# Kernel tuning notes

Hardware: AMD Instinct MI355X
Metric: run time of the kernel (lower is better)

## Reference

```python
import jax, jax.numpy as jnp
import numpy as np

B, N, C, H = 8, 1024, 1024, 16
DH = C // H
SCALE = DH ** -0.5
EPS = 1e-6


def layernorm(x, g, b):
    m = jnp.mean(x, axis=-1, keepdims=True)
    v = jnp.mean(jnp.square(x - m), axis=-1, keepdims=True)
    return (x - m) * jax.lax.rsqrt(v + EPS) * g + b


def setup_inputs() -> dict:
    key = jax.random.key(0)
    ks = jax.random.split(key, 5)
    w = 0.02  # init std for weights, keeps activations sane
    return {
        "x": jax.random.normal(ks[0], (B, N, C), jnp.float32),
        "qkv_w": jax.random.normal(ks[1], (C, 3 * C), jnp.float32) * w,
        "qkv_b": jnp.zeros((3 * C,), jnp.float32),
        "proj_w": jax.random.normal(ks[2], (C, C), jnp.float32) * w,
        "proj_b": jnp.zeros((C,), jnp.float32),
        "n1_g": jnp.ones((C,), jnp.float32),
        "n1_b": jnp.zeros((C,), jnp.float32),
        "fc1_w": jax.random.normal(ks[3], (C, 4 * C), jnp.float32) * w,
        "fc1_b": jnp.zeros((4 * C,), jnp.float32),
        "fc2_w": jax.random.normal(ks[4], (4 * C, C), jnp.float32) * w,
        "fc2_b": jnp.zeros((C,), jnp.float32),
        "n2_g": jnp.ones((C,), jnp.float32),
        "n2_b": jnp.zeros((C,), jnp.float32),
    }


def reference(x, qkv_w, qkv_b, proj_w, proj_b, n1_g, n1_b,
              fc1_w, fc1_b, fc2_w, fc2_b, n2_g, n2_b):
    # --- manual multi-head attention (timm-style, materializes BxHxNxN) ---
    qkv = x @ qkv_w + qkv_b                                  # [B,N,3C]
    qkv = qkv.reshape(B, N, 3, H, DH).transpose(2, 0, 3, 1, 4)  # [3,B,H,N,DH]
    q, k, v = qkv[0], qkv[1], qkv[2]
    attn = jax.nn.softmax(jnp.einsum('bhnd,bhmd->bhnm', q, k) * SCALE, axis=-1)
    y = jnp.einsum('bhnm,bhmd->bhnd', attn, v)               # [B,H,N,DH]
    y = y.transpose(0, 2, 1, 3).reshape(B, N, C)
    y = y @ proj_w + proj_b                                  # attention output replaces x
    # --- NOTE: unusual block wiring, faithful to source ---
    # x = attn_out; x = x + norm1(x); x = x + norm2(mlp(x))
    y = y + layernorm(y, n1_g, n1_b)
    h = jax.nn.gelu(y @ fc1_w + fc1_b, approximate=False)    # timm Mlp: fc1 -> GELU -> fc2
    h = h @ fc2_w + fc2_b
    y = y + layernorm(h, n2_g, n2_b)
    return y
```

## Files before the change

### kernel.cpp

```cpp
#include <hip/hip_runtime.h>
#include <hip/hip_bf16.h>
#include <math.h>

typedef __bf16 bf16;
typedef __bf16 bf16x8 __attribute__((ext_vector_type(8)));
typedef float f32x4 __attribute__((ext_vector_type(4)));

__device__ __forceinline__ int swz_idx(int row, int col) {
    return ((row) << 6) + (((((col) >> 3) ^ ((row) & 7)) << 3) | ((col) & 7));
}
#define LDS_SWZ8(row, c8) ((((row)) << 6) + ((((c8) ^ ((row) & 7))) << 3))

__device__ __forceinline__ void gload_lds16(const bf16* g, bf16* l) {
    __builtin_amdgcn_global_load_lds(
        (const __attribute__((address_space(1))) void*)g,
        (__attribute__((address_space(3))) void*)l,
        16, 0, 0);
}

template <int ROWS>
__device__ __forceinline__ void stage_swz(const bf16* __restrict__ src, long rstride,
                                          bf16* lds, int tid) {
#pragma unroll
    for (int pass = 0; pass < ROWS / 32; ++pass) {
        int e = pass * 2048 + tid * 8;
        int r = e >> 6;
        int c8 = (e >> 3) & 7;
        int sc8 = c8 ^ (r & 7);
        gload_lds16(src + (long)r * rstride + sc8 * 8, lds + e);
    }
}

__global__ void transpose_cvt(const float* __restrict__ src, bf16* __restrict__ dst,
                              int R, int C) {
    __shared__ float tile[32][33];
    int bx = blockIdx.x * 32;
    int by = blockIdx.y * 32;
    int tx = threadIdx.x, ty = threadIdx.y;
#pragma unroll
    for (int j = 0; j < 32; j += 8)
        tile[ty + j][tx] = src[(long)(by + ty + j) * C + bx + tx];
    __syncthreads();
#pragma unroll
    for (int j = 0; j < 32; j += 8)
        dst[(long)(bx + ty + j) * R + by + tx] = (bf16)tile[tx][ty + j];
}

__global__ void cvt_bf16_kernel(const float* __restrict__ src, bf16* __restrict__ dst,
                                long n) {
    long i = ((long)blockIdx.x * blockDim.x + threadIdx.x) * 4;
    if (i < n) {
        float4 v = *(const float4*)(src + i);
        short4 pk;
        pk.x = (short)__builtin_bit_cast(unsigned short, (bf16)v.x);
        pk.y = (short)__builtin_bit_cast(unsigned short, (bf16)v.y);
        pk.z = (short)__builtin_bit_cast(unsigned short, (bf16)v.z);
        pk.w = (short)__builtin_bit_cast(unsigned short, (bf16)v.w);
        *(short4*)(dst + i) = pk;
    }
}

template <int MODE>
__global__ __launch_bounds__(256, 2)
void gemm_bt(const bf16* __restrict__ A, const bf16* __restrict__ Bt,
             const float* __restrict__ bias,
             float* __restrict__ Cf, bf16* __restrict__ Cb0,
             bf16* __restrict__ Cb1, bf16* __restrict__ Cb2,
             int M, int N, int K) {
    __shared__ __align__(16) bf16 lsA[128 * 64];
    __shared__ __align__(16) bf16 lsB[128 * 64];

    const int tid = threadIdx.x;
    const int lane = tid & 63;
    const int w = tid >> 6;
    const int wm = w >> 1, wn = w & 1;
    const int l15 = lane & 15, l4 = lane >> 4;
    const int row0 = blockIdx.y * 128;
    const int col0 = blockIdx.x * 128;

    f32x4 acc[4][4] = {};

    for (int k0 = 0; k0 < K; k0 += 64) {
        stage_swz<128>(A + (long)row0 * K + k0, K, lsA, tid);
        stage_swz<128>(Bt + (long)col0 * K + k0, K, lsB, tid);
        __syncthreads();
#pragma unroll
        for (int kk = 0; kk < 2; ++kk) {
            int c8 = kk * 4 + l4;
            bf16x8 af[4], bfr[4];
#pragma unroll
            for (int mt = 0; mt < 4; ++mt)
                af[mt] = *(const bf16x8*)(&lsA[LDS_SWZ8(wm * 64 + mt * 16 + l15, c8)]);
#pragma unroll
            for (int nt = 0; nt < 4; ++nt)
                bfr[nt] = *(const bf16x8*)(&lsB[LDS_SWZ8(wn * 64 + nt * 16 + l15, c8)]);
#pragma unroll
            for (int mt = 0; mt < 4; ++mt)
#pragma unroll
                for (int nt = 0; nt < 4; ++nt)
                    acc[mt][nt] = __builtin_amdgcn_mfma_f32_16x16x32_bf16(
                        af[mt], bfr[nt], acc[mt][nt], 0, 0, 0);
        }
        __syncthreads();
    }

#pragma unroll
    for (int mt = 0; mt < 4; ++mt) {
#pragma unroll
        for (int nt = 0; nt < 4; ++nt) {
            int colb = col0 + wn * 64 + nt * 16 + l15;
            float bv = bias[colb];
#pragma unroll
            for (int i = 0; i < 4; ++i) {
                int row = row0 + wm * 64 + mt * 16 + l4 * 4 + i;
                int col = colb;
                float v = acc[mt][nt][i] + bv;
                if (MODE == 0) {
                    int b = row >> 10, nn = row & 1023;
                    int s = col >> 10, rem = col & 1023;
                    int h = rem >> 6, d = rem & 63;
                    long bh = (long)b * 16 + h;
                    if (s == 0)      Cb0[(bh * 1024 + nn) * 64 + d] = (bf16)(v * 0.125f);
                    else if (s == 1) Cb1[(bh * 1024 + nn) * 64 + d] = (bf16)v;
                    else             Cb2[(bh * 64 + d) * 1024 + nn] = (bf16)v;
                } else if (MODE == 1) {
                    Cf[(long)row * N + col] = v;
                } else if (MODE == 2) {
                    float g = 0.5f * v * (1.0f + erff(v * 0.70710678118f));
                    Cb0[(long)row * N + col] = (bf16)g;
                } else {
                    Cf[(long)row * N + col] = v;
                }
            }
        }
    }
}

__global__ __launch_bounds__(256, 2)
void attn_flash(const bf16* __restrict__ Q, const bf16* __restrict__ Kv,
                const bf16* __restrict__ Vt, bf16* __restrict__ Y) {
    __shared__ __align__(16) bf16 lsK[2][64 * 64];
    __shared__ __align__(16) bf16 lsV[2][64 * 64];
    __shared__ __align__(16) bf16 lsP[4][16 * 64];

    const int tid = threadIdx.x;
    const int lane = tid & 63;
    const int w = tid >> 6;
    const int l15 = lane & 15, l4 = lane >> 4;
    const int bh = blockIdx.y;
    const int b = bh >> 4, h = bh & 15;
    const int q0 = blockIdx.x * 64;

    const bf16* qp = Q + ((long)bh * 1024 + q0 + w * 16 + l15) * 64;
    bf16x8 qa[2];
    qa[0] = *(const bf16x8*)(qp + 8 * l4);
    qa[1] = *(const bf16x8*)(qp + 32 + 8 * l4);

    const bf16* kbase = Kv + (long)bh * 1024 * 64;
    const bf16* vbase = Vt + (long)bh * 64 * 1024;

    float lsum[4] = {0.f, 0.f, 0.f, 0.f};
    f32x4 oacc[4] = {};

    stage_swz<64>(kbase, 64, lsK[0], tid);
    stage_swz<64>(vbase, 1024, lsV[0], tid);
    __syncthreads();

    for (int t = 0; t < 16; ++t) {
        const int cur = t & 1;
        if (t < 15) {
            int kv0 = (t + 1) * 64;
            stage_swz<64>(kbase + (long)kv0 * 64, 64, lsK[cur ^ 1], tid);
            stage_swz<64>(vbase + kv0, 1024, lsV[cur ^ 1], tid);
        }

        f32x4 s[4] = {};
#pragma unroll
        for (int kk = 0; kk < 2; ++kk) {
            int c8 = kk * 4 + l4;
#pragma unroll
            for (int nt = 0; nt < 4; ++nt) {
                bf16x8 kb = *(const bf16x8*)(&lsK[cur][LDS_SWZ8(nt * 16 + l15, c8)]);
                s[nt] = __builtin_amdgcn_mfma_f32_16x16x32_bf16(qa[kk], kb, s[nt], 0, 0, 0);
            }
        }

#pragma unroll
        for (int i = 0; i < 4; ++i) {
            int prow = l4 * 4 + i;
#pragma unroll
            for (int nt = 0; nt < 4; ++nt) {
                float p = __expf(s[nt][i]);
                lsum[i] += p;
                lsP[w][swz_idx(prow, nt * 16 + l15)] = (bf16)p;
            }
        }
        __builtin_amdgcn_sched_barrier(0);
        asm volatile("s_waitcnt lgkmcnt(0)" ::: "memory");
        __builtin_amdgcn_sched_barrier(0);

#pragma unroll
        for (int kk = 0; kk < 2; ++kk) {
            int c8 = kk * 4 + l4;
            bf16x8 pa = *(const bf16x8*)(&lsP[w][LDS_SWZ8(l15, c8)]);
#pragma unroll
            for (int nt = 0; nt < 4; ++nt) {
                bf16x8 vb = *(const bf16x8*)(&lsV[cur][LDS_SWZ8(nt * 16 + l15, c8)]);
                oacc[nt] = __builtin_amdgcn_mfma_f32_16x16x32_bf16(pa, vb, oacc[nt], 0, 0, 0);
            }
        }
        __syncthreads();
    }

#pragma unroll
    for (int i = 0; i < 4; ++i) {
#pragma unroll
        for (int off = 1; off < 16; off <<= 1)
            lsum[i] += __shfl_xor(lsum[i], off);
    }

#pragma unroll
    for (int i = 0; i < 4; ++i) {
        float rinv = 1.0f / lsum[i];
        int row = q0 + w * 16 + l4 * 4 + i;
#pragma unroll
        for (int nt = 0; nt < 4; ++nt) {
            int d = nt * 16 + l15;
            Y[((long)b * 1024 + row) * 1024 + h * 64 + d] = (bf16)(oacc[nt][i] * rinv);
        }
    }
}

__device__ __forceinline__ float block_reduce_sum(float v, float* sm) {
#pragma unroll
    for (int off = 1; off < 64; off <<= 1) v += __shfl_xor(v, off);
    int w = threadIdx.x >> 6;
    if ((threadIdx.x & 63) == 0) sm[w] = v;
    __syncthreads();
    v = sm[0] + sm[1] + sm[2] + sm[3];
    __syncthreads();
    return v;
}

__global__ __launch_bounds__(256)
void res_ln(float* __restrict__ Yf, bf16* __restrict__ Yb,
            const float* __restrict__ g, const float* __restrict__ beta) {
    __shared__ float sm[4];
    const long row = blockIdx.x;
    float* p = Yf + row * 1024;
    const int t = threadIdx.x;
    float4 x = *(const float4*)(p + t * 4);
    float s = x.x + x.y + x.z + x.w;
    s = block_reduce_sum(s, sm);
    float mean = s * (1.0f / 1024.0f);
    float d0 = x.x - mean, d1 = x.y - mean, d2 = x.z - mean, d3 = x.w - mean;
    float sq = d0 * d0 + d1 * d1 + d2 * d2 + d3 * d3;
    sq = block_reduce_sum(sq, sm);
    float rs = rsqrtf(sq * (1.0f / 1024.0f) + 1e-6f);
    float4 gg = *(const float4*)(g + t * 4);
    float4 bb = *(const float4*)(beta + t * 4);
    float o0 = x.x + d0 * rs * gg.x + bb.x;
    float o1 = x.y + d1 * rs * gg.y + bb.y;
    float o2 = x.z + d2 * rs * gg.z + bb.z;
    float o3 = x.w + d3 * rs * gg.w + bb.w;
    *(float4*)(p + t * 4) = make_float4(o0, o1, o2, o3);
    short4 pk;
    pk.x = (short)__builtin_bit_cast(unsigned short, (bf16)o0);
    pk.y = (short)__builtin_bit_cast(unsigned short, (bf16)o1);
    pk.z = (short)__builtin_bit_cast(unsigned short, (bf16)o2);
    pk.w = (short)__builtin_bit_cast(unsigned short, (bf16)o3);
    *(short4*)(Yb + row * 1024 + t * 4) = pk;
}

__global__ __launch_bounds__(256)
void final_ln(float* __restrict__ Hf, const float* __restrict__ Yres,
              const float* __restrict__ g, const float* __restrict__ beta) {
    __shared__ float sm[4];
    const long row = blockIdx.x;
    float* p = Hf + row * 1024;
    const float* yr = Yres + row * 1024;
    const int t = threadIdx.x;
    float4 x = *(const float4*)(p + t * 4);
    float s = x.x + x.y + x.z + x.w;
    s = block_reduce_sum(s, sm);
    float mean = s * (1.0f / 1024.0f);
    float d0 = x.x - mean, d1 = x.y - mean, d2 = x.z - mean, d3 = x.w - mean;
    float sq = d0 * d0 + d1 * d1 + d2 * d2 + d3 * d3;
    sq = block_reduce_sum(sq, sm);
    float rs = rsqrtf(sq * (1.0f / 1024.0f) + 1e-6f);
    float4 gg = *(const float4*)(g + t * 4);
    float4 bb = *(const float4*)(beta + t * 4);
    float4 y = *(const float4*)(yr + t * 4);
    float4 o;
    o.x = y.x + d0 * rs * gg.x + bb.x;
    o.y = y.y + d1 * rs * gg.y + bb.y;
    o.z = y.z + d2 * rs * gg.z + bb.z;
    o.w = y.w + d3 * rs * gg.w + bb.w;
    *(float4*)(p + t * 4) = o;
}

extern "C" void kernel_launch(void* const* d_in, const int* in_sizes, int n_in,
                              void* d_out, int out_size, void* d_ws, size_t ws_size,
                              hipStream_t stream) {
    const float* x      = (const float*)d_in[0];
    const float* qkv_w  = (const float*)d_in[1];
    const float* qkv_b  = (const float*)d_in[2];
    const float* proj_w = (const float*)d_in[3];
    const float* proj_b = (const float*)d_in[4];
    const float* n1_g   = (const float*)d_in[5];
    const float* n1_b   = (const float*)d_in[6];
    const float* fc1_w  = (const float*)d_in[7];
    const float* fc1_b  = (const float*)d_in[8];
    const float* fc2_w  = (const float*)d_in[9];
    const float* fc2_b  = (const float*)d_in[10];
    const float* n2_g   = (const float*)d_in[11];
    const float* n2_b   = (const float*)d_in[12];

    char* ws = (char*)d_ws;
    const long MB = 1l << 20;
    bf16*  qkvT  = (bf16*)(ws + 0 * MB);
    bf16*  projT = (bf16*)(ws + 6 * MB);
    bf16*  fc1T  = (bf16*)(ws + 8 * MB);
    bf16*  fc2T  = (bf16*)(ws + 16 * MB);
    bf16*  xbf   = (bf16*)(ws + 24 * MB);
    bf16*  yattn = (bf16*)(ws + 24 * MB);
    bf16*  qb    = (bf16*)(ws + 40 * MB);
    bf16*  kb    = (bf16*)(ws + 56 * MB);
    bf16*  vtb   = (bf16*)(ws + 72 * MB);
    float* yproj = (float*)(ws + 40 * MB);
    bf16*  yresb = (bf16*)(ws + 72 * MB);
    bf16*  h1    = (bf16*)(ws + 88 * MB);
    float* outf  = (float*)d_out;

    dim3 tb(32, 8);
    transpose_cvt<<<dim3(3072 / 32, 1024 / 32), tb, 0, stream>>>(qkv_w, qkvT, 1024, 3072);
    transpose_cvt<<<dim3(1024 / 32, 1024 / 32), tb, 0, stream>>>(proj_w, projT, 1024, 1024);
    transpose_cvt<<<dim3(4096 / 32, 1024 / 32), tb, 0, stream>>>(fc1_w, fc1T, 1024, 4096);
    transpose_cvt<<<dim3(1024 / 32, 4096 / 32), tb, 0, stream>>>(fc2_w, fc2T, 4096, 1024);
    cvt_bf16_kernel<<<8192, 256, 0, stream>>>(x, xbf, 8388608);

    gemm_bt<0><<<dim3(3072 / 128, 8192 / 128), 256, 0, stream>>>(
        xbf, qkvT, qkv_b, nullptr, qb, kb, vtb, 8192, 3072, 1024);
    attn_flash<<<dim3(1024 / 64, 128), 256, 0, stream>>>(qb, kb, vtb, yattn);
    gemm_bt<1><<<dim3(1024 / 128, 8192 / 128), 256, 0, stream>>>(
        yattn, projT, proj_b, yproj, nullptr, nullptr, nullptr, 8192, 1024, 1024);
    res_ln<<<8192, 256, 0, stream>>>(yproj, yresb, n1_g, n1_b);
    gemm_bt<2><<<dim3(4096 / 128, 8192 / 128), 256, 0, stream>>>(
        yresb, fc1T, fc1_b, nullptr, h1, nullptr, nullptr, 8192, 4096, 1024);
    gemm_bt<3><<<dim3(1024 / 128, 8192 / 128), 256, 0, stream>>>(
        h1, fc2T, fc2_b, outf, nullptr, nullptr, nullptr, 8192, 1024, 4096);
    final_ln<<<8192, 256, 0, stream>>>(outf, yproj, n2_g, n2_b);
}
```

Baseline: 385.5 us.

## Replace GEMM with double-buffered 256x128 tile kernel with split-K-plane prefetch

Rewrites all four linear-layer GEMMs as a 512-thread, 256x128-tile kernel. It double-buffers LDS in two 32-wide K half-planes and issues the global-to-LDS loads for the next tile while MFMAs run on the current one. It also adds workgroup index swizzling for L2 locality, a new XOR swizzle for the 32-column planes, and s_setprio around the MFMA block. The aim is to hide global load latency, which the old single-buffered load/sync/compute loop exposed, at the cost of more LDS (96KB per block) and hand-tuned waitcnt and barrier synchronization.

```diff
diff --git a/kernel.cpp b/kernel.cpp
--- a/kernel.cpp
+++ b/kernel.cpp
@@ -5,11 +5,6 @@
 typedef __bf16 bf16;
 typedef __bf16 bf16x8 __attribute__((ext_vector_type(8)));
 typedef float f32x4 __attribute__((ext_vector_type(4)));
-
-__device__ __forceinline__ int swz_idx(int row, int col) {
-    return ((row) << 6) + (((((col) >> 3) ^ ((row) & 7)) << 3) | ((col) & 7));
-}
-#define LDS_SWZ8(row, c8) ((((row)) << 6) + ((((c8) ^ ((row) & 7))) << 3))
 
 __device__ __forceinline__ void gload_lds16(const bf16* g, bf16* l) {
     __builtin_amdgcn_global_load_lds(
@@ -17,6 +12,28 @@
         (__attribute__((address_space(3))) void*)l,
         16, 0, 0);
 }
+
+__device__ __forceinline__ int plane_idx(int row, int c4) {
+    return row * 32 + (((c4) ^ ((row >> 1) & 3)) << 3);
+}
+
+template <int ISSUES>
+__device__ __forceinline__ void stage_plane(const bf16* __restrict__ gbase, long rstride,
+                                            bf16* plane, int tid) {
+#pragma unroll
+    for (int j = 0; j < ISSUES; ++j) {
+        int e = j * 4096 + tid * 8;
+        int r = e >> 5;
+        int c4 = (e >> 3) & 3;
+        int cs = c4 ^ ((r >> 1) & 3);
+        gload_lds16(gbase + (long)r * rstride + cs * 8, plane + e);
+    }
+}
+
+__device__ __forceinline__ int swz_idx(int row, int col) {
+    return ((row) << 6) + (((((col) >> 3) ^ ((row) & 7)) << 3) | ((col) & 7));
+}
+#define LDS_SWZ8(row, c8) ((((row)) << 6) + ((((c8) ^ ((row) & 7))) << 3))
 
 template <int ROWS>
 __device__ __forceinline__ void stage_swz(const bf16* __restrict__ src, long rstride,
@@ -61,60 +78,117 @@
 }
 
 template <int MODE>
-__global__ __launch_bounds__(256, 2)
-void gemm_bt(const bf16* __restrict__ A, const bf16* __restrict__ Bt,
-             const float* __restrict__ bias,
-             float* __restrict__ Cf, bf16* __restrict__ Cb0,
-             bf16* __restrict__ Cb1, bf16* __restrict__ Cb2,
-             int M, int N, int K) {
-    __shared__ __align__(16) bf16 lsA[128 * 64];
-    __shared__ __align__(16) bf16 lsB[128 * 64];
+__global__ __launch_bounds__(512, 2)
+void gemm_8ph(const bf16* __restrict__ A, const bf16* __restrict__ Bt,
+              const float* __restrict__ bias,
+              float* __restrict__ Cf, bf16* __restrict__ Cb0,
+              bf16* __restrict__ Cb1, bf16* __restrict__ Cb2,
+              int M, int N, int K) {
+    __shared__ __align__(16) bf16 lsA[2][2][256 * 32];
+    __shared__ __align__(16) bf16 lsB[2][2][128 * 32];
+
+    const int nwg = gridDim.x * gridDim.y;
+    const int lin = blockIdx.y * gridDim.x + blockIdx.x;
+    const int swz = (lin & 7) * (nwg >> 3) + (lin >> 3);
+    const int bx = swz % gridDim.x, by = swz / gridDim.x;
+    const int brow = by * 256, bcol = bx * 128;
 
     const int tid = threadIdx.x;
     const int lane = tid & 63;
-    const int w = tid >> 6;
-    const int wm = w >> 1, wn = w & 1;
+    const int wid = tid >> 6;
+    const int wm = wid >> 1, wn = wid & 1;
     const int l15 = lane & 15, l4 = lane >> 4;
-    const int row0 = blockIdx.y * 128;
-    const int col0 = blockIdx.x * 128;
-
+
+    const int NT = K >> 6;
     f32x4 acc[4][4] = {};
 
-    for (int k0 = 0; k0 < K; k0 += 64) {
-        stage_swz<128>(A + (long)row0 * K + k0, K, lsA, tid);
-        stage_swz<128>(Bt + (long)col0 * K + k0, K, lsB, tid);
-        __syncthreads();
+    const bf16* Abase = A + (long)brow * K;
+    const bf16* Bbase = Bt + (long)bcol * K;
+
+    stage_plane<2>(Abase, K, lsA[0][0], tid);
+    stage_plane<1>(Bbase, K, lsB[0][0], tid);
+    stage_plane<2>(Abase + 32, K, lsA[0][1], tid);
+    stage_plane<1>(Bbase + 32, K, lsB[0][1], tid);
+    asm volatile("s_waitcnt vmcnt(3)" ::: "memory");
+    __builtin_amdgcn_s_barrier();
+    __builtin_amdgcn_sched_barrier(0);
+
+    for (int t = 0; t < NT - 1; ++t) {
+        const int bf = t & 1;
+        const bf16* An = Abase + (t + 1) * 64;
+        const bf16* Bn = Bbase + (t + 1) * 64;
 #pragma unroll
         for (int kk = 0; kk < 2; ++kk) {
-            int c8 = kk * 4 + l4;
-            bf16x8 af[4], bfr[4];
-#pragma unroll
-            for (int mt = 0; mt < 4; ++mt)
-                af[mt] = *(const bf16x8*)(&lsA[LDS_SWZ8(wm * 64 + mt * 16 + l15, c8)]);
-#pragma unroll
-            for (int nt = 0; nt < 4; ++nt)
-                bfr[nt] = *(const bf16x8*)(&lsB[LDS_SWZ8(wn * 64 + nt * 16 + l15, c8)]);
-#pragma unroll
-            for (int mt = 0; mt < 4; ++mt)
-#pragma unroll
-                for (int nt = 0; nt < 4; ++nt)
-                    acc[mt][nt] = __builtin_amdgcn_mfma_f32_16x16x32_bf16(
-                        af[mt], bfr[nt], acc[mt][nt], 0, 0, 0);
-        }
-        __syncthreads();
-    }
-
-#pragma unroll
-    for (int mt = 0; mt < 4; ++mt) {
-#pragma unroll
-        for (int nt = 0; nt < 4; ++nt) {
-            int colb = col0 + wn * 64 + nt * 16 + l15;
+            bf16x8 aF[4], bF[4];
+            const bf16* pA = lsA[bf][kk];
+            const bf16* pB = lsB[bf][kk];
+#pragma unroll
+            for (int m = 0; m < 4; ++m)
+                aF[m] = *(const bf16x8*)(pA + plane_idx(wm * 64 + m * 16 + l15, l4));
+#pragma unroll
+            for (int n = 0; n < 4; ++n)
+                bF[n] = *(const bf16x8*)(pB + plane_idx(wn * 64 + n * 16 + l15, l4));
+            stage_plane<2>(An + kk * 32, K, lsA[bf ^ 1][kk], tid);
+            stage_plane<1>(Bn + kk * 32, K, lsB[bf ^ 1][kk], tid);
+            __builtin_amdgcn_s_barrier();
+            asm volatile("s_waitcnt lgkmcnt(0)" ::: "memory");
+            __builtin_amdgcn_sched_barrier(0);
+            __builtin_amdgcn_s_setprio(1);
+#pragma unroll
+            for (int m = 0; m < 4; ++m)
+#pragma unroll
+                for (int n = 0; n < 4; ++n)
+                    acc[m][n] = __builtin_amdgcn_mfma_f32_16x16x32_bf16(
+                        aF[m], bF[n], acc[m][n], 0, 0, 0);
+            __builtin_amdgcn_s_setprio(0);
+            __builtin_amdgcn_sched_barrier(0);
+            asm volatile("s_waitcnt vmcnt(3)" ::: "memory");
+            __builtin_amdgcn_s_barrier();
+            __builtin_amdgcn_sched_barrier(0);
+        }
+    }
+    {
+        const int bf = (NT - 1) & 1;
+#pragma unroll
+        for (int kk = 0; kk < 2; ++kk) {
+            bf16x8 aF[4], bF[4];
+            const bf16* pA = lsA[bf][kk];
+            const bf16* pB = lsB[bf][kk];
+#pragma unroll
+            for (int m = 0; m < 4; ++m)
+                aF[m] = *(const bf16x8*)(pA + plane_idx(wm * 64 + m * 16 + l15, l4));
+#pragma unroll
+            for (int n = 0; n < 4; ++n)
+                bF[n] = *(const bf16x8*)(pB + plane_idx(wn * 64 + n * 16 + l15, l4));
+            __builtin_amdgcn_s_barrier();
+            asm volatile("s_waitcnt lgkmcnt(0)" ::: "memory");
+            __builtin_amdgcn_sched_barrier(0);
+            __builtin_amdgcn_s_setprio(1);
+#pragma unroll
+            for (int m = 0; m < 4; ++m)
+#pragma unroll
+                for (int n = 0; n < 4; ++n)
+                    acc[m][n] = __builtin_amdgcn_mfma_f32_16x16x32_bf16(
+                        aF[m], bF[n], acc[m][n], 0, 0, 0);
+            __builtin_amdgcn_s_setprio(0);
+            __builtin_amdgcn_sched_barrier(0);
+            asm volatile("s_waitcnt vmcnt(0)" ::: "memory");
+            __builtin_amdgcn_s_barrier();
+            __builtin_amdgcn_sched_barrier(0);
+        }
+    }
+
+#pragma unroll
+    for (int m = 0; m < 4; ++m) {
+#pragma unroll
+        for (int n = 0; n < 4; ++n) {
+            int colb = bcol + wn * 64 + n * 16 + l15;
             float bv = bias[colb];
 #pragma unroll
             for (int i = 0; i < 4; ++i) {
-                int row = row0 + wm * 64 + mt * 16 + l4 * 4 + i;
+                int row = brow + wm * 64 + m * 16 + l4 * 4 + i;
                 int col = colb;
-                float v = acc[mt][nt][i] + bv;
+                float v = acc[m][n][i] + bv;
                 if (MODE == 0) {
                     int b = row >> 10, nn = row & 1023;
                     int s = col >> 10, rem = col & 1023;
@@ -339,15 +413,15 @@
     transpose_cvt<<<dim3(1024 / 32, 4096 / 32), tb, 0, stream>>>(fc2_w, fc2T, 4096, 1024);
     cvt_bf16_kernel<<<8192, 256, 0, stream>>>(x, xbf, 8388608);
 
-    gemm_bt<0><<<dim3(3072 / 128, 8192 / 128), 256, 0, stream>>>(
+    gemm_8ph<0><<<dim3(3072 / 128, 8192 / 256), 512, 0, stream>>>(
         xbf, qkvT, qkv_b, nullptr, qb, kb, vtb, 8192, 3072, 1024);
     attn_flash<<<dim3(1024 / 64, 128), 256, 0, stream>>>(qb, kb, vtb, yattn);
-    gemm_bt<1><<<dim3(1024 / 128, 8192 / 128), 256, 0, stream>>>(
+    gemm_8ph<1><<<dim3(1024 / 128, 8192 / 256), 512, 0, stream>>>(
         yattn, projT, proj_b, yproj, nullptr, nullptr, nullptr, 8192, 1024, 1024);
     res_ln<<<8192, 256, 0, stream>>>(yproj, yresb, n1_g, n1_b);
-    gemm_bt<2><<<dim3(4096 / 128, 8192 / 128), 256, 0, stream>>>(
+    gemm_8ph<2><<<dim3(4096 / 128, 8192 / 256), 512, 0, stream>>>(
         yresb, fc1T, fc1_b, nullptr, h1, nullptr, nullptr, 8192, 4096, 1024);
-    gemm_bt<3><<<dim3(1024 / 128, 8192 / 128), 256, 0, stream>>>(
+    gemm_8ph<3><<<dim3(1024 / 128, 8192 / 256), 512, 0, stream>>>(
         h1, fc2T, fc2_b, outf, nullptr, nullptr, nullptr, 8192, 1024, 4096);
     final_ln<<<8192, 256, 0, stream>>>(outf, yproj, n2_g, n2_b);
 }
```

New measurement: 433.2 us. 12.4% more time.

## Replace GEMM with double-buffered 256x128 phased pipeline kernel

Applied to the files above, without the earlier changes.

Replaces the single-buffered 128x128 GEMM with a 512-thread 256x128 tile kernel. It double-buffers LDS in two 32-wide K halves, issuing the global-to-LDS loads for the next tile while the MFMAs run on the current one, under explicit waitcnt, barrier and setprio scheduling. It also remaps workgroup IDs to improve L2 locality and uses a new XOR swizzle for the LDS reads. This is meant to hide global load latency and the per-iteration sync stalls. In exchange it uses more LDS and fragile hand-tuned synchronisation, and K is fixed as a template parameter.

```diff
diff --git a/kernel.cpp b/kernel.cpp
--- a/kernel.cpp
+++ b/kernel.cpp
@@ -5,11 +5,6 @@
 typedef __bf16 bf16;
 typedef __bf16 bf16x8 __attribute__((ext_vector_type(8)));
 typedef float f32x4 __attribute__((ext_vector_type(4)));
-
-__device__ __forceinline__ int swz_idx(int row, int col) {
-    return ((row) << 6) + (((((col) >> 3) ^ ((row) & 7)) << 3) | ((col) & 7));
-}
-#define LDS_SWZ8(row, c8) ((((row)) << 6) + ((((c8) ^ ((row) & 7))) << 3))
 
 __device__ __forceinline__ void gload_lds16(const bf16* g, bf16* l) {
     __builtin_amdgcn_global_load_lds(
@@ -17,6 +12,11 @@
         (__attribute__((address_space(3))) void*)l,
         16, 0, 0);
 }
+
+__device__ __forceinline__ int swz_idx(int row, int col) {
+    return ((row) << 6) + (((((col) >> 3) ^ ((row) & 7)) << 3) | ((col) & 7));
+}
+#define LDS_SWZ8(row, c8) ((((row)) << 6) + ((((c8) ^ ((row) & 7))) << 3))
 
 template <int ROWS>
 __device__ __forceinline__ void stage_swz(const bf16* __restrict__ src, long rstride,
@@ -60,61 +60,137 @@
     }
 }
 
-template <int MODE>
-__global__ __launch_bounds__(256, 2)
-void gemm_bt(const bf16* __restrict__ A, const bf16* __restrict__ Bt,
-             const float* __restrict__ bias,
-             float* __restrict__ Cf, bf16* __restrict__ Cb0,
-             bf16* __restrict__ Cb1, bf16* __restrict__ Cb2,
-             int M, int N, int K) {
-    __shared__ __align__(16) bf16 lsA[128 * 64];
-    __shared__ __align__(16) bf16 lsB[128 * 64];
+template <int MODE, int KT>
+__global__ __launch_bounds__(512, 2)
+void gemm_8ph(const bf16* __restrict__ A, const bf16* __restrict__ Bt,
+              const float* __restrict__ bias,
+              float* __restrict__ Cf, bf16* __restrict__ Cb0,
+              bf16* __restrict__ Cb1, bf16* __restrict__ Cb2,
+              int M, int N) {
+    __shared__ __align__(16) bf16 lsA[2][2][256 * 32];
+    __shared__ __align__(16) bf16 lsB[2][2][128 * 32];
+
+    constexpr int NT = KT / 64;
+    static_assert(((NT - 1) & 1) == 1, "main loop tile count must be odd");
+    constexpr int PAIRS = (NT - 1) / 2;
+
+    const int nwg = gridDim.x * gridDim.y;
+    const int lin = blockIdx.y * gridDim.x + blockIdx.x;
+    const int swz = (lin & 7) * (nwg >> 3) + (lin >> 3);
+    const int bx = swz % gridDim.x, by = swz / gridDim.x;
+    const int brow = by * 256, bcol = bx * 128;
 
     const int tid = threadIdx.x;
     const int lane = tid & 63;
-    const int w = tid >> 6;
-    const int wm = w >> 1, wn = w & 1;
+    const int wid = tid >> 6;
+    const int wm = wid >> 1, wn = wid & 1;
     const int l15 = lane & 15, l4 = lane >> 4;
-    const int row0 = blockIdx.y * 128;
-    const int col0 = blockIdx.x * 128;
 
     f32x4 acc[4][4] = {};
 
-    for (int k0 = 0; k0 < K; k0 += 64) {
-        stage_swz<128>(A + (long)row0 * K + k0, K, lsA, tid);
-        stage_swz<128>(Bt + (long)col0 * K + k0, K, lsB, tid);
-        __syncthreads();
-#pragma unroll
-        for (int kk = 0; kk < 2; ++kk) {
-            int c8 = kk * 4 + l4;
-            bf16x8 af[4], bfr[4];
-#pragma unroll
-            for (int mt = 0; mt < 4; ++mt)
-                af[mt] = *(const bf16x8*)(&lsA[LDS_SWZ8(wm * 64 + mt * 16 + l15, c8)]);
-#pragma unroll
-            for (int nt = 0; nt < 4; ++nt)
-                bfr[nt] = *(const bf16x8*)(&lsB[LDS_SWZ8(wn * 64 + nt * 16 + l15, c8)]);
-#pragma unroll
-            for (int mt = 0; mt < 4; ++mt)
-#pragma unroll
-                for (int nt = 0; nt < 4; ++nt)
-                    acc[mt][nt] = __builtin_amdgcn_mfma_f32_16x16x32_bf16(
-                        af[mt], bfr[nt], acc[mt][nt], 0, 0, 0);
-        }
-        __syncthreads();
-    }
-
-#pragma unroll
-    for (int mt = 0; mt < 4; ++mt) {
-#pragma unroll
-        for (int nt = 0; nt < 4; ++nt) {
-            int colb = col0 + wn * 64 + nt * 16 + l15;
+    const int xorkey = (l4 ^ ((l15 >> 1) & 3)) << 3;
+    const int abyte = ((wm * 64 + l15) * 32 + xorkey) * 2;
+    const int bbyte = ((wn * 64 + l15) * 32 + xorkey) * 2;
+    const char* lsAc = (const char*)&lsA[0][0][0];
+    const char* lsBc = (const char*)&lsB[0][0][0];
+
+    const int tid4 = tid >> 2;
+    const int cs8 = (((tid & 3) ^ ((tid >> 3) & 3))) * 8;
+    const bf16* gA0 = A + (long)(brow + tid4) * KT + cs8;
+    const bf16* gA1 = gA0 + (long)128 * KT;
+    const bf16* gB0 = Bt + (long)(bcol + tid4) * KT + cs8;
+    const int tid8 = tid * 8;
+
+    gload_lds16(gA0,      &lsA[0][0][tid8]);
+    gload_lds16(gA1,      &lsA[0][0][tid8 + 4096]);
+    gload_lds16(gB0,      &lsB[0][0][tid8]);
+    gload_lds16(gA0 + 32, &lsA[0][1][tid8]);
+    gload_lds16(gA1 + 32, &lsA[0][1][tid8 + 4096]);
+    gload_lds16(gB0 + 32, &lsB[0][1][tid8]);
+    gA0 += 64; gA1 += 64; gB0 += 64;
+    asm volatile("s_waitcnt vmcnt(3)" ::: "memory");
+    __builtin_amdgcn_s_barrier();
+    __builtin_amdgcn_sched_barrier(0);
+
+#define DS_READS(bfc, kkc)                                                        \
+    bf16x8 aF[4], bF[4];                                                          \
+    _Pragma("unroll")                                                             \
+    for (int m = 0; m < 4; ++m)                                                   \
+        aF[m] = *(const bf16x8*)(lsAc + ((bfc) * 32768 + (kkc) * 16384 + m * 1024) + abyte); \
+    _Pragma("unroll")                                                             \
+    for (int n = 0; n < 4; ++n)                                                   \
+        bF[n] = *(const bf16x8*)(lsBc + ((bfc) * 16384 + (kkc) * 8192 + n * 1024) + bbyte);
+
+#define MFMA16()                                                                  \
+    __builtin_amdgcn_s_setprio(1);                                                \
+    _Pragma("unroll")                                                             \
+    for (int m = 0; m < 4; ++m)                                                   \
+        _Pragma("unroll")                                                         \
+        for (int n = 0; n < 4; ++n)                                               \
+            acc[m][n] = __builtin_amdgcn_mfma_f32_16x16x32_bf16(aF[m], bF[n],     \
+                                                                acc[m][n], 0, 0, 0); \
+    __builtin_amdgcn_s_setprio(0);                                                \
+    __builtin_amdgcn_sched_barrier(0);
+
+#define PHASE(bfc, kkc)                                                           \
+    do {                                                                          \
+        DS_READS(bfc, kkc)                                                        \
+        gload_lds16(gA0 + (kkc) * 32, &lsA[(bfc) ^ 1][kkc][tid8]);                \
+        gload_lds16(gA1 + (kkc) * 32, &lsA[(bfc) ^ 1][kkc][tid8 + 4096]);         \
+        gload_lds16(gB0 + (kkc) * 32, &lsB[(bfc) ^ 1][kkc][tid8]);                \
+        __builtin_amdgcn_s_barrier();                                             \
+        asm volatile("s_waitcnt lgkmcnt(0)" ::: "memory");                        \
+        __builtin_amdgcn_sched_barrier(0);                                        \
+        MFMA16()                                                                  \
+        asm volatile("s_waitcnt vmcnt(3)" ::: "memory");                          \
+        __builtin_amdgcn_s_barrier();                                             \
+        __builtin_amdgcn_sched_barrier(0);                                        \
+    } while (0)
+
+#define PHASE_LAST(bfc, kkc)                                                      \
+    do {                                                                          \
+        DS_READS(bfc, kkc)                                                        \
+        __builtin_amdgcn_s_barrier();                                             \
+        asm volatile("s_waitcnt lgkmcnt(0)" ::: "memory");                        \
+        __builtin_amdgcn_sched_barrier(0);                                        \
+        MFMA16()                                                                  \
+        asm volatile("s_waitcnt vmcnt(0)" ::: "memory");                          \
+        __builtin_amdgcn_s_barrier();                                             \
+        __builtin_amdgcn_sched_barrier(0);                                        \
+    } while (0)
+
+#define TILE(bfc)                                                                 \
+    do {                                                                          \
+        PHASE(bfc, 0);                                                            \
+        PHASE(bfc, 1);                                                            \
+        gA0 += 64; gA1 += 64; gB0 += 64;                                          \
+    } while (0)
+
+    for (int tp = 0; tp < PAIRS; ++tp) {
+        TILE(0);
+        TILE(1);
+    }
+    TILE(0);
+    PHASE_LAST(1, 0);
+    PHASE_LAST(1, 1);
+
+#undef TILE
+#undef PHASE
+#undef PHASE_LAST
+#undef MFMA16
+#undef DS_READS
+
+#pragma unroll
+    for (int m = 0; m < 4; ++m) {
+#pragma unroll
+        for (int n = 0; n < 4; ++n) {
+            int colb = bcol + wn * 64 + n * 16 + l15;
             float bv = bias[colb];
 #pragma unroll
             for (int i = 0; i < 4; ++i) {
-                int row = row0 + wm * 64 + mt * 16 + l4 * 4 + i;
+                int row = brow + wm * 64 + m * 16 + l4 * 4 + i;
                 int col = colb;
-                float v = acc[mt][nt][i] + bv;
+                float v = acc[m][n][i] + bv;
                 if (MODE == 0) {
                     int b = row >> 10, nn = row & 1023;
                     int s = col >> 10, rem = col & 1023;
@@ -339,15 +415,15 @@
     transpose_cvt<<<dim3(1024 / 32, 4096 / 32), tb, 0, stream>>>(fc2_w, fc2T, 4096, 1024);
     cvt_bf16_kernel<<<8192, 256, 0, stream>>>(x, xbf, 8388608);
 
-    gemm_bt<0><<<dim3(3072 / 128, 8192 / 128), 256, 0, stream>>>(
-        xbf, qkvT, qkv_b, nullptr, qb, kb, vtb, 8192, 3072, 1024);
+    gemm_8ph<0, 1024><<<dim3(3072 / 128, 8192 / 256), 512, 0, stream>>>(
+        xbf, qkvT, qkv_b, nullptr, qb, kb, vtb, 8192, 3072);
     attn_flash<<<dim3(1024 / 64, 128), 256, 0, stream>>>(qb, kb, vtb, yattn);
-    gemm_bt<1><<<dim3(1024 / 128, 8192 / 128), 256, 0, stream>>>(
-        yattn, projT, proj_b, yproj, nullptr, nullptr, nullptr, 8192, 1024, 1024);
+    gemm_8ph<1, 1024><<<dim3(1024 / 128, 8192 / 256), 512, 0, stream>>>(
+        yattn, projT, proj_b, yproj, nullptr, nullptr, nullptr, 8192, 1024);
     res_ln<<<8192, 256, 0, stream>>>(yproj, yresb, n1_g, n1_b);
-    gemm_bt<2><<<dim3(4096 / 128, 8192 / 128), 256, 0, stream>>>(
-        yresb, fc1T, fc1_b, nullptr, h1, nullptr, nullptr, 8192, 4096, 1024);
-    gemm_bt<3><<<dim3(1024 / 128, 8192 / 128), 256, 0, stream>>>(
-        h1, fc2T, fc2_b, outf, nullptr, nullptr, nullptr, 8192, 1024, 4096);
+    gemm_8ph<2, 1024><<<dim3(4096 / 128, 8192 / 256), 512, 0, stream>>>(
+        yresb, fc1T, fc1_b, nullptr, h1, nullptr, nullptr, 8192, 4096);
+    gemm_8ph<3, 4096><<<dim3(1024 / 128, 8192 / 256), 512, 0, stream>>>(
+        h1, fc2T, fc2_b, outf, nullptr, nullptr, nullptr, 8192, 1024);
     final_ln<<<8192, 256, 0, stream>>>(outf, yproj, n2_g, n2_b);
 }
```

Result: slower. 452.5 us (+17.4%).
